# Performance work log

Hardware: AMD Instinct MI355X
Metric: run time of the kernel (lower is better)

The kernel has to match this reference:

```python
import jax, jax.numpy as jnp
import numpy as np


def setup_inputs() -> dict:
    key = jax.random.key(0)
    ks = jax.random.split(key, 5)
    B, N, Fin, Fout = 8, 2048, 512, 512
    stdv = 1.0 / np.sqrt(Fout)
    w_stdv = 1.0 / np.sqrt(Fin)
    x = jax.random.normal(ks[0], (B, N, Fin), dtype=jnp.float32)
    weight = jax.random.uniform(ks[1], (Fin, Fout), dtype=jnp.float32, minval=-stdv, maxval=stdv)
    bias = jax.random.uniform(ks[2], (Fout,), dtype=jnp.float32, minval=-stdv, maxval=stdv)
    w_one = jax.random.uniform(ks[3], (Fin, Fin), dtype=jnp.float32, minval=-w_stdv, maxval=w_stdv)
    w_two = jax.random.uniform(ks[4], (Fin, Fin), dtype=jnp.float32, minval=-w_stdv, maxval=w_stdv)
    return {"x": x, "weight": weight, "bias": bias, "w_one": w_one, "w_two": w_two}


def reference(x, weight, bias, w_one, w_two):
    # x: [B, N, Fin]
    support = jnp.einsum('bnf,fo->bno', x, weight)          # [B, N, Fout]
    phi_one = jnp.einsum('ef,bnf->ben', w_one, x)           # [B, Fin, N]
    phi_two = jnp.einsum('ef,bnf->ben', w_two, x)           # [B, Fin, N]
    adj = jnp.einsum('ben,bem->bnm', phi_one, phi_two)      # [B, N, N]
    adj = jax.nn.softmax(adj, axis=1)                        # softmax over dim=1 (columns)
    out = jnp.einsum('bnm,bmo->bno', adj, support)           # [B, N, Fout]
    return out + bias
```

## Files before the change

### kernel.cpp

```cpp
#include <hip/hip_runtime.h>
#include <math.h>

#define BB 8
#define NN 2048
#define FF 512
#define LOG2E 1.4426950408889634f

typedef __attribute__((ext_vector_type(8))) short short8;
typedef __attribute__((ext_vector_type(4))) float floatx4;
typedef __attribute__((ext_vector_type(2))) float float2v;
typedef __attribute__((ext_vector_type(2))) __bf16 bf16x2;

__device__ __forceinline__ unsigned short f2bf(float f) {
    union { float f; unsigned u; } v; v.f = f;
    unsigned r = v.u + 0x7FFFu + ((v.u >> 16) & 1u);
    return (unsigned short)(r >> 16);
}

__device__ __forceinline__ float fexp2(float x) {
#if __has_builtin(__builtin_amdgcn_exp2f)
    return __builtin_amdgcn_exp2f(x);
#else
    return __expf(x * 0.69314718056f);
#endif
}

__device__ __forceinline__ void pk_store(unsigned short* p0, unsigned short* p1,
                                         float a, float b) {
    union { bf16x2 h; unsigned short s[2]; } u;
    float2v v; v.x = a; v.y = b;
    u.h = __builtin_convertvector(v, bf16x2);
    *p0 = u.s[0]; *p1 = u.s[1];
}

__global__ __launch_bounds__(256) void gemm_mfma_bt(
    const unsigned short* __restrict__ A, const unsigned short* __restrict__ B,
    void* __restrict__ Cv, const float* __restrict__ bias, float* __restrict__ Dsum,
    int M, int Nc, int K, int a_ld, int b_ld, int ldc,
    long a_batch, long b_batch, long c_batch, int mode)
{
    __shared__ __align__(16) unsigned short Alds[128 * 64];
    __shared__ __align__(16) unsigned short Blds[128 * 64];

    const int tid  = threadIdx.x;
    const int wave = tid >> 6;
    const int lane = tid & 63;
    const int bz   = blockIdx.z;

    const int m0 = blockIdx.y * 128;
    const int n0 = blockIdx.x * 128;

    const unsigned short* Aptr = A + (long)bz * a_batch + (long)m0 * a_ld;
    const unsigned short* Bptr = B + (long)bz * b_batch + (long)n0 * b_ld;

    const int wm   = (wave >> 1) * 64;
    const int wn   = (wave & 1) * 64;
    const int fl   = lane & 15;
    const int quad = lane >> 4;

    int offA[4], offB[4], cb[4];
    #pragma unroll
    for (int issue = 0; issue < 4; ++issue) {
        const int cbase = issue * 256 + wave * 64;
        const int c = cbase + lane;
        const int row = c >> 3;
        const int kq = ((c & 7) ^ ((c >> 3) & 7)) * 8;
        offA[issue] = row * a_ld + kq;
        offB[issue] = row * b_ld + kq;
        cb[issue] = cbase * 8;
    }

    floatx4 acc[4][4] = {};

    for (int k0 = 0; k0 < K; k0 += 64) {
        #pragma unroll
        for (int issue = 0; issue < 4; ++issue) {
            __builtin_amdgcn_global_load_lds(
                (const __attribute__((address_space(1))) void*)(Aptr + offA[issue]),
                (__attribute__((address_space(3))) void*)&Alds[cb[issue]], 16, 0, 0);
            __builtin_amdgcn_global_load_lds(
                (const __attribute__((address_space(1))) void*)(Bptr + offB[issue]),
                (__attribute__((address_space(3))) void*)&Blds[cb[issue]], 16, 0, 0);
        }
        Aptr += 64; Bptr += 64;
        __syncthreads();

        #pragma unroll
        for (int s = 0; s < 2; ++s) {
            short8 af[4], bf[4];
            const int slot = ((s * 4 + quad) ^ (fl & 7)) * 8;
            #pragma unroll
            for (int i = 0; i < 4; ++i)
                af[i] = *(const short8*)&Alds[(wm + i * 16 + fl) * 64 + slot];
            #pragma unroll
            for (int j = 0; j < 4; ++j)
                bf[j] = *(const short8*)&Blds[(wn + j * 16 + fl) * 64 + slot];
            #pragma unroll
            for (int i = 0; i < 4; ++i)
                #pragma unroll
                for (int j = 0; j < 4; ++j)
                    acc[i][j] = __builtin_amdgcn_mfma_f32_16x16x32_bf16(af[i], bf[j], acc[i][j], 0, 0, 0);
        }
        __syncthreads();
    }

    if (mode == 0) {
        float* Cb = (float*)Cv + (long)bz * c_batch;
        #pragma unroll
        for (int j = 0; j < 4; ++j) {
            const int ng = n0 + wn + j * 16 + fl;
            const float badd = bias ? bias[ng] : 0.0f;
            #pragma unroll
            for (int i = 0; i < 4; ++i) {
                const int mg = m0 + wm + i * 16 + quad * 4;
                #pragma unroll
                for (int r = 0; r < 4; ++r)
                    Cb[(long)(mg + r) * ldc + ng] = acc[i][j][r] + badd;
            }
        }
    } else if (mode == 1) {
        unsigned short* Cb = (unsigned short*)Cv + (long)bz * c_batch;
        #pragma unroll
        for (int j = 0; j < 4; ++j) {
            const int ng = n0 + wn + j * 16 + fl;
            #pragma unroll
            for (int i = 0; i < 4; ++i) {
                const int mg = m0 + wm + i * 16 + quad * 4;
                pk_store(&Cb[(long)(mg + 0) * ldc + ng], &Cb[(long)(mg + 1) * ldc + ng],
                         acc[i][j][0], acc[i][j][1]);
                pk_store(&Cb[(long)(mg + 2) * ldc + ng], &Cb[(long)(mg + 3) * ldc + ng],
                         acc[i][j][2], acc[i][j][3]);
            }
        }
    } else {
        unsigned short* Cb = (unsigned short*)Cv + (long)bz * c_batch;
        float* Db = Dsum + (long)bz * NN;
        #pragma unroll
        for (int i = 0; i < 4; ++i)
            #pragma unroll
            for (int j = 0; j < 4; ++j)
                #pragma unroll
                for (int r = 0; r < 4; ++r)
                    acc[i][j][r] = fexp2(acc[i][j][r]);
        #pragma unroll
        for (int j = 0; j < 4; ++j) {
            const int ng = n0 + wn + j * 16 + fl;
            float csum = 0.f;
            #pragma unroll
            for (int i = 0; i < 4; ++i) {
                const int mg = m0 + wm + i * 16 + quad * 4;
                csum += acc[i][j][0] + acc[i][j][1] + acc[i][j][2] + acc[i][j][3];
                pk_store(&Cb[(long)(mg + 0) * ldc + ng], &Cb[(long)(mg + 1) * ldc + ng],
                         acc[i][j][0], acc[i][j][1]);
                pk_store(&Cb[(long)(mg + 2) * ldc + ng], &Cb[(long)(mg + 3) * ldc + ng],
                         acc[i][j][2], acc[i][j][3]);
            }
            csum += __shfl_xor(csum, 16);
            csum += __shfl_xor(csum, 32);
            if (quad == 0) atomicAdd(&Db[ng], csum);
        }
    }
}

__global__ __launch_bounds__(256) void convert_all(
    const float* __restrict__ x, const float* __restrict__ w1, const float* __restrict__ w2,
    unsigned short* __restrict__ xb, unsigned short* __restrict__ w1b, unsigned short* __restrict__ w2b)
{
    const long NX = (long)BB * NN * FF / 8;
    const long NW = (long)FF * FF / 8;
    long t = (long)blockIdx.x * 256 + threadIdx.x;
    const float* in; unsigned short* out; float sc = 1.0f;
    if (t < NX) { in = x; out = xb; }
    else if (t < NX + NW) { in = w1; out = w1b; t -= NX; sc = LOG2E; }
    else if (t < NX + 2 * NW) { in = w2; out = w2b; t -= NX + NW; }
    else return;
    const long i = t * 8;
    float4 a = *(const float4*)(in + i);
    float4 b = *(const float4*)(in + i + 4);
    union { bf16x2 h[4]; short8 s8; } u;
    float2v v;
    v.x = a.x * sc; v.y = a.y * sc; u.h[0] = __builtin_convertvector(v, bf16x2);
    v.x = a.z * sc; v.y = a.w * sc; u.h[1] = __builtin_convertvector(v, bf16x2);
    v.x = b.x * sc; v.y = b.y * sc; u.h[2] = __builtin_convertvector(v, bf16x2);
    v.x = b.z * sc; v.y = b.w * sc; u.h[3] = __builtin_convertvector(v, bf16x2);
    *(short8*)(out + i) = u.s8;
}

__global__ __launch_bounds__(256) void transpose_convert(
    const float* __restrict__ in, unsigned short* __restrict__ out, int dim)
{
    __shared__ float t[32][33];
    const int tx = threadIdx.x & 31, ty = threadIdx.x >> 5;
    const int x0 = blockIdx.x * 32, y0 = blockIdx.y * 32;
    #pragma unroll
    for (int k = 0; k < 32; k += 8)
        t[ty + k][tx] = in[(long)(y0 + ty + k) * dim + x0 + tx];
    __syncthreads();
    #pragma unroll
    for (int k = 0; k < 32; k += 8)
        out[(long)(x0 + ty + k) * dim + y0 + tx] = f2bf(t[tx][ty + k]);
}

__global__ __launch_bounds__(256) void zero_f32(float* __restrict__ p, long n)
{
    long i = (long)blockIdx.x * 256 + threadIdx.x;
    if (i < n) p[i] = 0.0f;
}

__global__ __launch_bounds__(256) void scale_transpose(
    const unsigned short* __restrict__ Call, const float* __restrict__ D,
    unsigned short* __restrict__ supT, int batch0)
{
    __shared__ float t[32][33];
    __shared__ float rD[32];
    const int tx = threadIdx.x & 31, ty = threadIdx.x >> 5;
    const int mt = blockIdx.x * 32, ot = blockIdx.y * 32;
    const int b = batch0 + blockIdx.z;
    const unsigned short* Cb = Call + (long)b * NN * 1536;
    unsigned short* Tb = supT + (long)b * NN * FF;
    if (threadIdx.x < 32) rD[threadIdx.x] = 1.0f / D[(long)b * NN + mt + threadIdx.x];
    __syncthreads();
    #pragma unroll
    for (int k = 0; k < 32; k += 8) {
        unsigned short u = Cb[(long)(mt + ty + k) * 1536 + 1024 + ot + tx];
        union { unsigned uu; float f; } cv; cv.uu = ((unsigned)u) << 16;
        t[ty + k][tx] = cv.f;
    }
    __syncthreads();
    #pragma unroll
    for (int k = 0; k < 32; k += 8)
        Tb[(long)(ot + ty + k) * NN + mt + tx] = f2bf(t[tx][ty + k] * rD[tx]);
}

extern "C" void kernel_launch(void* const* d_in, const int* in_sizes, int n_in,
                              void* d_out, int out_size, void* d_ws, size_t ws_size,
                              hipStream_t stream)
{
    const float* x      = (const float*)d_in[0];
    const float* weight = (const float*)d_in[1];
    const float* bias   = (const float*)d_in[2];
    const float* w_one  = (const float*)d_in[3];
    const float* w_two  = (const float*)d_in[4];
    float* out = (float*)d_out;

    const long NF  = (long)NN * FF;
    const long NN2 = (long)NN * NN;
    const long CROW = 1536;

    char* p = (char*)d_ws;
    unsigned short* xb    = (unsigned short*)p; p += (size_t)BB * NF * 2;
    unsigned short* Wall  = (unsigned short*)p; p += (size_t)CROW * FF * 2;
    unsigned short* Call  = (unsigned short*)p; p += (size_t)BB * NN * CROW * 2;
    unsigned short* supT  = (unsigned short*)p; p += (size_t)BB * NF * 2;
    float*          Dsum  = (float*)p;          p += (size_t)BB * NN * 4;
    unsigned short* E     = (unsigned short*)p;
    unsigned short* w1b = Wall;
    unsigned short* w2b = Wall + (size_t)FF * FF;
    unsigned short* wTb = Wall + (size_t)2 * FF * FF;

    const size_t fixed = (size_t)(p - (char*)d_ws);
    const bool full = ws_size >= fixed + (size_t)BB * NN2 * 2;

    dim3 blk(256);

    convert_all<<<dim3(4352), blk, 0, stream>>>(x, w_one, w_two, xb, w1b, w2b);
    transpose_convert<<<dim3(FF / 32, FF / 32), blk, 0, stream>>>(weight, wTb, FF);
    zero_f32<<<dim3((BB * NN) / 256), blk, 0, stream>>>(Dsum, BB * NN);

    gemm_mfma_bt<<<dim3(CROW / 128, NN / 128, BB), blk, 0, stream>>>(
        xb, Wall, Call, nullptr, nullptr, NN, (int)CROW, FF,
        FF, FF, (int)CROW, NF, 0, NN * CROW, 1);

    if (full) {
        gemm_mfma_bt<<<dim3(NN / 128, NN / 128, BB), blk, 0, stream>>>(
            Call, Call + FF, E, nullptr, Dsum, NN, NN, FF,
            (int)CROW, (int)CROW, NN, NN * CROW, NN * CROW, NN2, 2);
        scale_transpose<<<dim3(NN / 32, FF / 32, BB), blk, 0, stream>>>(Call, Dsum, supT, 0);
        gemm_mfma_bt<<<dim3(FF / 128, NN / 128, BB), blk, 0, stream>>>(
            E, supT, out, bias, nullptr, NN, FF, NN,
            NN, NN, FF, NN2, NF, NF, 0);
    } else {
        for (int b = 0; b < BB; ++b) {
            const unsigned short* Cb = Call + (size_t)b * NN * CROW;
            gemm_mfma_bt<<<dim3(NN / 128, NN / 128, 1), blk, 0, stream>>>(
                Cb, Cb + FF, E, nullptr, Dsum + (size_t)b * NN, NN, NN, FF,
                (int)CROW, (int)CROW, NN, 0, 0, 0, 2);
            scale_transpose<<<dim3(NN / 32, FF / 32, 1), blk, 0, stream>>>(Call, Dsum, supT, b);
            gemm_mfma_bt<<<dim3(FF / 128, NN / 128, 1), blk, 0, stream>>>(
                E, supT + (size_t)b * NF, out + (size_t)b * NF, bias, nullptr, NN, FF, NN,
                NN, NN, FF, 0, 0, 0, 0);
        }
    }
}
```

Before: 241.8 us.

## Replace GEMM with 256-row tiled, triple-buffered, 512-thread templated MFMA kernel

Replaces the 128x128 single-buffered bf16 MFMA GEMM with a templated kernel using 256xBN tiles, 8 waves, and a 3-stage LDS ring over K=32 slices. Global-to-LDS loads are issued two stages ahead, with explicit vmcnt waits and barriers, so load latency overlaps MFMA work. Larger per-wave tiles (8xNR fragments) increase data reuse per LDS read. The mode branch becomes a template parameter so the compiler can specialise each epilogue. The cost is higher register pressure from the larger accumulator array, fewer blocks per GEMM which may leave CUs idle on the smaller GEMMs, and hand-tuned waitcnt counts that must exactly match the number of loads issued.

```diff
diff --git a/kernel.cpp b/kernel.cpp
--- a/kernel.cpp
+++ b/kernel.cpp
@@ -33,127 +33,173 @@
     *p0 = u.s[0]; *p1 = u.s[1];
 }
 
-__global__ __launch_bounds__(256) void gemm_mfma_bt(
+template<int BN_T, int MODE>
+__global__ __launch_bounds__(512, 2) void gemm256_bt(
     const unsigned short* __restrict__ A, const unsigned short* __restrict__ B,
     void* __restrict__ Cv, const float* __restrict__ bias, float* __restrict__ Dsum,
     int M, int Nc, int K, int a_ld, int b_ld, int ldc,
-    long a_batch, long b_batch, long c_batch, int mode)
-{
-    __shared__ __align__(16) unsigned short Alds[128 * 64];
-    __shared__ __align__(16) unsigned short Blds[128 * 64];
+    long a_batch, long b_batch, long c_batch)
+{
+    constexpr int NR    = BN_T / 64;
+    constexpr int B_ISS = BN_T / 128;
+
+    __shared__ __align__(16) unsigned short Alds[3][256 * 32];
+    __shared__ __align__(16) unsigned short Blds[3][BN_T * 32];
 
     const int tid  = threadIdx.x;
     const int wave = tid >> 6;
     const int lane = tid & 63;
+    const int wr   = wave >> 2;
+    const int wc   = wave & 3;
+    const int fl   = lane & 15;
+    const int quad = lane >> 4;
     const int bz   = blockIdx.z;
 
-    const int m0 = blockIdx.y * 128;
-    const int n0 = blockIdx.x * 128;
+    const int m0 = blockIdx.y * 256;
+    const int n0 = blockIdx.x * BN_T;
 
     const unsigned short* Aptr = A + (long)bz * a_batch + (long)m0 * a_ld;
     const unsigned short* Bptr = B + (long)bz * b_batch + (long)n0 * b_ld;
 
-    const int wm   = (wave >> 1) * 64;
-    const int wn   = (wave & 1) * 64;
-    const int fl   = lane & 15;
-    const int quad = lane >> 4;
-
-    int offA[4], offB[4], cb[4];
-    #pragma unroll
-    for (int issue = 0; issue < 4; ++issue) {
-        const int cbase = issue * 256 + wave * 64;
-        const int c = cbase + lane;
-        const int row = c >> 3;
-        const int kq = ((c & 7) ^ ((c >> 3) & 7)) * 8;
-        offA[issue] = row * a_ld + kq;
-        offB[issue] = row * b_ld + kq;
-        cb[issue] = cbase * 8;
-    }
-
-    floatx4 acc[4][4] = {};
-
-    for (int k0 = 0; k0 < K; k0 += 64) {
-        #pragma unroll
-        for (int issue = 0; issue < 4; ++issue) {
+    int offA[2], offB[B_ISS];
+    #pragma unroll
+    for (int i = 0; i < 2; ++i) {
+        const int cl = i * 512 + tid;
+        const int L = cl >> 3, s = cl & 7;
+        const int cc = s ^ (L & 7);
+        offA[i] = (2 * L + (cc >> 2)) * a_ld + (cc & 3) * 8;
+    }
+    #pragma unroll
+    for (int i = 0; i < B_ISS; ++i) {
+        const int cl = i * 512 + tid;
+        const int L = cl >> 3, s = cl & 7;
+        const int cc = s ^ (L & 7);
+        offB[i] = (2 * L + (cc >> 2)) * b_ld + (cc & 3) * 8;
+    }
+
+    const int slot = (quad | ((fl & 1) << 2)) ^ (fl >> 1);
+    const int aRd  = (wr * 64 + (fl >> 1)) * 64 + slot * 8;
+    const int bRd  = (wc * (BN_T / 8) + (fl >> 1)) * 64 + slot * 8;
+
+    auto STAGE = [&](int buf, const unsigned short* Ap, const unsigned short* Bp) {
+        #pragma unroll
+        for (int i = 0; i < 2; ++i)
             __builtin_amdgcn_global_load_lds(
-                (const __attribute__((address_space(1))) void*)(Aptr + offA[issue]),
-                (__attribute__((address_space(3))) void*)&Alds[cb[issue]], 16, 0, 0);
+                (const __attribute__((address_space(1))) void*)(Ap + offA[i]),
+                (__attribute__((address_space(3))) void*)&Alds[buf][(i * 512 + tid) * 8],
+                16, 0, 0);
+        #pragma unroll
+        for (int i = 0; i < B_ISS; ++i)
             __builtin_amdgcn_global_load_lds(
-                (const __attribute__((address_space(1))) void*)(Bptr + offB[issue]),
-                (__attribute__((address_space(3))) void*)&Blds[cb[issue]], 16, 0, 0);
-        }
-        Aptr += 64; Bptr += 64;
-        __syncthreads();
-
-        #pragma unroll
-        for (int s = 0; s < 2; ++s) {
-            short8 af[4], bf[4];
-            const int slot = ((s * 4 + quad) ^ (fl & 7)) * 8;
-            #pragma unroll
-            for (int i = 0; i < 4; ++i)
-                af[i] = *(const short8*)&Alds[(wm + i * 16 + fl) * 64 + slot];
-            #pragma unroll
-            for (int j = 0; j < 4; ++j)
-                bf[j] = *(const short8*)&Blds[(wn + j * 16 + fl) * 64 + slot];
-            #pragma unroll
-            for (int i = 0; i < 4; ++i)
-                #pragma unroll
-                for (int j = 0; j < 4; ++j)
-                    acc[i][j] = __builtin_amdgcn_mfma_f32_16x16x32_bf16(af[i], bf[j], acc[i][j], 0, 0, 0);
-        }
-        __syncthreads();
-    }
-
-    if (mode == 0) {
+                (const __attribute__((address_space(1))) void*)(Bp + offB[i]),
+                (__attribute__((address_space(3))) void*)&Blds[buf][(i * 512 + tid) * 8],
+                16, 0, 0);
+    };
+
+    floatx4 acc[8][NR] = {};
+
+    const int nt = K >> 5;
+    STAGE(0, Aptr, Bptr);
+    STAGE(1, Aptr + 32, Bptr + 32);
+    const unsigned short* Ast = Aptr + 64;
+    const unsigned short* Bst = Bptr + 64;
+    int rd = 0, st = 2;
+
+    for (int t = 0; t < nt; ++t) {
+        if (t + 2 < nt) {
+            STAGE(st, Ast, Bst);
+            Ast += 32; Bst += 32;
+            if constexpr (BN_T == 256) asm volatile("s_waitcnt vmcnt(8)" ::: "memory");
+            else                       asm volatile("s_waitcnt vmcnt(6)" ::: "memory");
+        } else if (t + 2 == nt) {
+            if constexpr (BN_T == 256) asm volatile("s_waitcnt vmcnt(4)" ::: "memory");
+            else                       asm volatile("s_waitcnt vmcnt(3)" ::: "memory");
+        } else {
+            asm volatile("s_waitcnt vmcnt(0)" ::: "memory");
+        }
+        __builtin_amdgcn_sched_barrier(0);
+        __builtin_amdgcn_s_barrier();
+        __builtin_amdgcn_sched_barrier(0);
+
+        const unsigned short* Ab = Alds[rd];
+        const unsigned short* Bb = Blds[rd];
+        short8 af[8], bfr[NR];
+        #pragma unroll
+        for (int m = 0; m < 8; ++m)
+            af[m] = *(const short8*)&Ab[aRd + m * 512];
+        #pragma unroll
+        for (int n = 0; n < NR; ++n)
+            bfr[n] = *(const short8*)&Bb[bRd + n * 512];
+
+        __builtin_amdgcn_s_setprio(1);
+        #pragma unroll
+        for (int m = 0; m < 8; ++m)
+            #pragma unroll
+            for (int n = 0; n < NR; ++n)
+                acc[m][n] = __builtin_amdgcn_mfma_f32_16x16x32_bf16(af[m], bfr[n], acc[m][n], 0, 0, 0);
+        __builtin_amdgcn_s_setprio(0);
+
+        __builtin_amdgcn_sched_barrier(0);
+        __builtin_amdgcn_s_barrier();
+        __builtin_amdgcn_sched_barrier(0);
+
+        rd = (rd == 2) ? 0 : rd + 1;
+        st = (st == 2) ? 0 : st + 1;
+    }
+
+    const int wmg = m0 + wr * 128;
+    const int wng = n0 + wc * (BN_T / 4);
+
+    if constexpr (MODE == 0) {
         float* Cb = (float*)Cv + (long)bz * c_batch;
         #pragma unroll
-        for (int j = 0; j < 4; ++j) {
-            const int ng = n0 + wn + j * 16 + fl;
+        for (int n = 0; n < NR; ++n) {
+            const int ng = wng + n * 16 + fl;
             const float badd = bias ? bias[ng] : 0.0f;
             #pragma unroll
-            for (int i = 0; i < 4; ++i) {
-                const int mg = m0 + wm + i * 16 + quad * 4;
+            for (int m = 0; m < 8; ++m) {
+                const int mg = wmg + m * 16 + quad * 4;
                 #pragma unroll
                 for (int r = 0; r < 4; ++r)
-                    Cb[(long)(mg + r) * ldc + ng] = acc[i][j][r] + badd;
+                    Cb[(long)(mg + r) * ldc + ng] = acc[m][n][r] + badd;
             }
         }
-    } else if (mode == 1) {
+    } else if constexpr (MODE == 1) {
         unsigned short* Cb = (unsigned short*)Cv + (long)bz * c_batch;
         #pragma unroll
-        for (int j = 0; j < 4; ++j) {
-            const int ng = n0 + wn + j * 16 + fl;
-            #pragma unroll
-            for (int i = 0; i < 4; ++i) {
-                const int mg = m0 + wm + i * 16 + quad * 4;
+        for (int n = 0; n < NR; ++n) {
+            const int ng = wng + n * 16 + fl;
+            #pragma unroll
+            for (int m = 0; m < 8; ++m) {
+                const int mg = wmg + m * 16 + quad * 4;
                 pk_store(&Cb[(long)(mg + 0) * ldc + ng], &Cb[(long)(mg + 1) * ldc + ng],
-                         acc[i][j][0], acc[i][j][1]);
+                         acc[m][n][0], acc[m][n][1]);
                 pk_store(&Cb[(long)(mg + 2) * ldc + ng], &Cb[(long)(mg + 3) * ldc + ng],
-                         acc[i][j][2], acc[i][j][3]);
+                         acc[m][n][2], acc[m][n][3]);
             }
         }
     } else {
         unsigned short* Cb = (unsigned short*)Cv + (long)bz * c_batch;
         float* Db = Dsum + (long)bz * NN;
         #pragma unroll
-        for (int i = 0; i < 4; ++i)
-            #pragma unroll
-            for (int j = 0; j < 4; ++j)
+        for (int m = 0; m < 8; ++m)
+            #pragma unroll
+            for (int n = 0; n < NR; ++n)
                 #pragma unroll
                 for (int r = 0; r < 4; ++r)
-                    acc[i][j][r] = fexp2(acc[i][j][r]);
-        #pragma unroll
-        for (int j = 0; j < 4; ++j) {
-            const int ng = n0 + wn + j * 16 + fl;
+                    acc[m][n][r] = fexp2(acc[m][n][r]);
+        #pragma unroll
+        for (int n = 0; n < NR; ++n) {
+            const int ng = wng + n * 16 + fl;
             float csum = 0.f;
             #pragma unroll
-            for (int i = 0; i < 4; ++i) {
-                const int mg = m0 + wm + i * 16 + quad * 4;
-                csum += acc[i][j][0] + acc[i][j][1] + acc[i][j][2] + acc[i][j][3];
+            for (int m = 0; m < 8; ++m) {
+                const int mg = wmg + m * 16 + quad * 4;
+                csum += acc[m][n][0] + acc[m][n][1] + acc[m][n][2] + acc[m][n][3];
                 pk_store(&Cb[(long)(mg + 0) * ldc + ng], &Cb[(long)(mg + 1) * ldc + ng],
-                         acc[i][j][0], acc[i][j][1]);
+                         acc[m][n][0], acc[m][n][1]);
                 pk_store(&Cb[(long)(mg + 2) * ldc + ng], &Cb[(long)(mg + 3) * ldc + ng],
-                         acc[i][j][2], acc[i][j][3]);
+                         acc[m][n][2], acc[m][n][3]);
             }
             csum += __shfl_xor(csum, 16);
             csum += __shfl_xor(csum, 32);
@@ -261,34 +307,34 @@
     const size_t fixed = (size_t)(p - (char*)d_ws);
     const bool full = ws_size >= fixed + (size_t)BB * NN2 * 2;
 
-    dim3 blk(256);
+    dim3 blk(256), blk5(512);
 
     convert_all<<<dim3(4352), blk, 0, stream>>>(x, w_one, w_two, xb, w1b, w2b);
     transpose_convert<<<dim3(FF / 32, FF / 32), blk, 0, stream>>>(weight, wTb, FF);
     zero_f32<<<dim3((BB * NN) / 256), blk, 0, stream>>>(Dsum, BB * NN);
 
-    gemm_mfma_bt<<<dim3(CROW / 128, NN / 128, BB), blk, 0, stream>>>(
+    gemm256_bt<128, 1><<<dim3(CROW / 128, NN / 256, BB), blk5, 0, stream>>>(
         xb, Wall, Call, nullptr, nullptr, NN, (int)CROW, FF,
-        FF, FF, (int)CROW, NF, 0, NN * CROW, 1);
+        FF, FF, (int)CROW, NF, 0, NN * CROW);
 
     if (full) {
-        gemm_mfma_bt<<<dim3(NN / 128, NN / 128, BB), blk, 0, stream>>>(
+        gemm256_bt<256, 2><<<dim3(NN / 256, NN / 256, BB), blk5, 0, stream>>>(
             Call, Call + FF, E, nullptr, Dsum, NN, NN, FF,
-            (int)CROW, (int)CROW, NN, NN * CROW, NN * CROW, NN2, 2);
+            (int)CROW, (int)CROW, NN, NN * CROW, NN * CROW, NN2);
         scale_transpose<<<dim3(NN / 32, FF / 32, BB), blk, 0, stream>>>(Call, Dsum, supT, 0);
-        gemm_mfma_bt<<<dim3(FF / 128, NN / 128, BB), blk, 0, stream>>>(
+        gemm256_bt<128, 0><<<dim3(FF / 128, NN / 256, BB), blk5, 0, stream>>>(
             E, supT, out, bias, nullptr, NN, FF, NN,
-            NN, NN, FF, NN2, NF, NF, 0);
+            NN, NN, FF, NN2, NF, NF);
     } else {
         for (int b = 0; b < BB; ++b) {
             const unsigned short* Cb = Call + (size_t)b * NN * CROW;
-            gemm_mfma_bt<<<dim3(NN / 128, NN / 128, 1), blk, 0, stream>>>(
+            gemm256_bt<256, 2><<<dim3(NN / 256, NN / 256, 1), blk5, 0, stream>>>(
                 Cb, Cb + FF, E, nullptr, Dsum + (size_t)b * NN, NN, NN, FF,
-                (int)CROW, (int)CROW, NN, 0, 0, 0, 2);
+                (int)CROW, (int)CROW, NN, 0, 0, 0);
             scale_transpose<<<dim3(NN / 32, FF / 32, 1), blk, 0, stream>>>(Call, Dsum, supT, b);
-            gemm_mfma_bt<<<dim3(FF / 128, NN / 128, 1), blk, 0, stream>>>(
+            gemm256_bt<128, 0><<<dim3(FF / 128, NN / 256, 1), blk5, 0, stream>>>(
                 E, supT + (size_t)b * NF, out + (size_t)b * NF, bias, nullptr, NN, FF, NN,
-                NN, NN, FF, 0, 0, 0, 0);
-        }
-    }
-}
+                NN, NN, FF, 0, 0, 0);
+        }
+    }
+}
```

After: 271.0 us. 12.1% more time.
